# Performance work log

Measured on AMD Instinct MI355X. Metric: run time of the kernel, lower is better.

## Reference

```python
import jax, jax.numpy as jnp
import numpy as np

D_MODEL = 256; D_FLOW = 128; D_FFN = 1024
N_HEADS = 8; N_LEVELS = 3; N_POINTS = 4
D_HEAD = D_MODEL // N_HEADS
SHAPES = np.array([[128, 128], [64, 64], [32, 32]], dtype=np.int64)


def setup_inputs():
    key = jax.random.key(0)
    ks = jax.random.split(key, 12)
    N = 2
    LeNin = int((SHAPES[:, 0] * SHAPES[:, 1]).sum())
    Lq = int(SHAPES[0, 0] * SHAPES[0, 1])
    lsi = np.concatenate([[0], np.cumsum(SHAPES[:, 0] * SHAPES[:, 1])[:-1]])
    s = 0.02
    return {
        'src': jax.random.normal(ks[0], (N, LeNin, D_MODEL), jnp.float32),
        'flow': jax.random.normal(ks[1], (N, Lq, D_FLOW), jnp.float32),
        'spatial_shapes': jnp.asarray(SHAPES, jnp.int32),
        'level_start_index': jnp.asarray(lsi, jnp.int32),
        'w_value': jax.random.normal(ks[2], (D_MODEL, D_MODEL), jnp.float32) * s,
        'b_value': jnp.zeros((D_MODEL,), jnp.float32),
        'w_off': jax.random.normal(ks[3], (D_FLOW, N_HEADS * N_LEVELS * N_POINTS * 2), jnp.float32) * s,
        'b_off': jax.random.normal(ks[4], (N_HEADS * N_LEVELS * N_POINTS * 2,), jnp.float32) * 0.5,
        'w_attn': jax.random.normal(ks[5], (D_FLOW, N_HEADS * N_LEVELS * N_POINTS), jnp.float32) * s,
        'b_attn': jnp.zeros((N_HEADS * N_LEVELS * N_POINTS,), jnp.float32),
        'w_out': jax.random.normal(ks[6], (D_MODEL, D_MODEL), jnp.float32) * s,
        'b_out': jnp.zeros((D_MODEL,), jnp.float32),
        'gamma': jnp.ones((D_MODEL,), jnp.float32),
        'beta': jnp.zeros((D_MODEL,), jnp.float32),
        'w1': jax.random.normal(ks[7], (D_MODEL, D_FFN), jnp.float32) * s,
        'b1': jnp.zeros((D_FFN,), jnp.float32),
        'w2': jax.random.normal(ks[8], (D_FFN, D_MODEL), jnp.float32) * s,
        'b2': jnp.zeros((D_MODEL,), jnp.float32),
    }


def _bilinear_level(v, xy, H, W):
    # v: [N, nh, H*W, dh]; xy: [N, Lq, nh, np, 2] normalized to [0,1]
    # grid_sample(align_corners=False) semantics: pixel = loc * size - 0.5, zero padding
    N, Lq = xy.shape[0], xy.shape[1]
    x = xy[..., 0] * W - 0.5
    y = xy[..., 1] * H - 0.5
    x0 = jnp.floor(x); y0 = jnp.floor(y)
    dx = x - x0; dy = y - y0
    acc = jnp.zeros((N, N_HEADS, Lq * N_POINTS, v.shape[-1]), v.dtype)
    corners = ((x0, y0, (1 - dx) * (1 - dy)),
               (x0 + 1, y0, dx * (1 - dy)),
               (x0, y0 + 1, (1 - dx) * dy),
               (x0 + 1, y0 + 1, dx * dy))
    for ix, iy, w in corners:
        valid = (ix >= 0) & (ix <= W - 1) & (iy >= 0) & (iy <= H - 1)
        xi = jnp.clip(ix, 0, W - 1).astype(jnp.int32)
        yi = jnp.clip(iy, 0, H - 1).astype(jnp.int32)
        idx = (yi * W + xi).transpose(0, 2, 1, 3).reshape(N, N_HEADS, Lq * N_POINTS)
        g = jnp.take_along_axis(v, idx[..., None], axis=2)  # [N, nh, Lq*np, dh]
        wv = (w * valid).transpose(0, 2, 1, 3).reshape(N, N_HEADS, Lq * N_POINTS, 1)
        acc = acc + wv * g
    return acc


def reference(src, flow, spatial_shapes, level_start_index, w_value, b_value,
              w_off, b_off, w_attn, b_attn, w_out, b_out, gamma, beta, w1, b1, w2, b2):
    ss = np.asarray(jax.device_get(spatial_shapes))
    lsi = np.asarray(jax.device_get(level_start_index))
    N, LeNin, _ = src.shape
    Lq = flow.shape[1]
    value = (src @ w_value + b_value).reshape(N, LeNin, N_HEADS, D_HEAD)
    off = (flow @ w_off + b_off).reshape(N, Lq, N_HEADS, N_LEVELS, N_POINTS, 2)
    attn = jax.nn.softmax((flow @ w_attn + b_attn).reshape(N, Lq, N_HEADS, N_LEVELS * N_POINTS), axis=-1)
    attn = attn.reshape(N, Lq, N_HEADS, N_LEVELS, N_POINTS)
    # reference points on level-0 grid (valid_ratios == 1)
    H0, W0 = int(ss[0, 0]), int(ss[0, 1])
    ry, rx = jnp.meshgrid(jnp.linspace(0.5, H0 - 0.5, H0) / H0,
                          jnp.linspace(0.5, W0 - 0.5, W0) / W0, indexing='ij')
    ref = jnp.stack([rx.reshape(-1), ry.reshape(-1)], -1)  # [Lq, 2] (x, y)
    norm = jnp.asarray(np.stack([ss[:, 1], ss[:, 0]], -1), jnp.float32)  # [nl, 2] = (W, H)
    loc = ref[None, :, None, None, None, :] + off / norm[None, None, None, :, None, :]
    acc = jnp.zeros((N, Lq, N_HEADS, D_HEAD), src.dtype)
    for l in range(N_LEVELS):
        H, W = int(ss[l, 0]), int(ss[l, 1])
        st = int(lsi[l])
        v = value[:, st:st + H * W].transpose(0, 2, 1, 3)  # [N, nh, HW, dh]
        s_l = _bilinear_level(v, loc[:, :, :, l], H, W).reshape(N, N_HEADS, Lq, N_POINTS, D_HEAD)
        acc = acc + jnp.einsum('bhqpd,bqhp->bqhd', s_l, attn[:, :, :, l])
    src2 = acc.reshape(N, Lq, D_MODEL) @ w_out + b_out
    x = src2  # dropout is identity at inference
    mu = x.mean(-1, keepdims=True)
    var = ((x - mu) ** 2).mean(-1, keepdims=True)
    ln = (x - mu) / jnp.sqrt(var + 1e-5) * gamma + beta
    ffn = jax.nn.relu(ln @ w1 + b1) @ w2 + b2
    return x + ffn
```

## Files before the change

### kernel.cpp

```cpp
#include <hip/hip_runtime.h>
#include <cstdint>
#include <cstddef>

#define D_MODEL  256
#define D_FLOW   128
#define D_FFN    1024
#define N_HEADS  8
#define N_LEVELS 3
#define N_POINTS 4
#define D_HEAD   32
#define LQ       16384
#define LENIN    21504
#define NB       2

typedef unsigned short ushort;
typedef __attribute__((ext_vector_type(8))) short bf16x8;
typedef __attribute__((ext_vector_type(4))) float f32x4;

__device__ __forceinline__ ushort f2b(float f) {
    uint32_t u = __float_as_uint(f);
    uint32_t r = (u + 0x7fffu + ((u >> 16) & 1u)) >> 16;
    return (ushort)r;
}

__device__ __forceinline__ void gl_lds16(const void* g, void* l) {
    __builtin_amdgcn_global_load_lds(
        (const __attribute__((address_space(1))) unsigned int*)g,
        (__attribute__((address_space(3))) unsigned int*)l,
        16, 0, 0);
}

template<bool A_FP32, bool RELU, bool RESID, bool OUT_BF16>
__global__ __launch_bounds__(256)
void mfma_gemm(const void* __restrict__ Ain, const ushort* __restrict__ Bt,
               const float* __restrict__ bias, const float* __restrict__ resid,
               void* __restrict__ Cout, int N, int K)
{
    __shared__ ushort As[128 * 64];
    __shared__ ushort Bs[128 * 64];

    const int tid  = threadIdx.x;
    const int wave = tid >> 6;
    const int lane = tid & 63;
    const int quad = lane >> 4;
    const int l16  = lane & 15;
    const int wr   = (wave >> 1) * 64;
    const int wc   = (wave & 1) * 64;

    const int nx = gridDim.x;
    int lin = blockIdx.y * nx + blockIdx.x;
    const int total = nx * gridDim.y;
    if ((total & 7) == 0) lin = (lin & 7) * (total >> 3) + (lin >> 3);
    const int by = lin / nx;
    const int bx = lin - by * nx;
    const int bm = by * 128;
    const int bn = bx * 128;

    const int sr  = lane >> 3;
    const int sc  = lane & 7;
    const int gch = sc ^ sr;

    f32x4 acc[4][4] = {};
    const int swz = l16 & 7;

    for (int k0 = 0; k0 < K; k0 += 64) {
        __syncthreads();
        if (A_FP32) {
            const float* Af = (const float*)Ain;
#pragma unroll
            for (int i = 0; i < 4; ++i) {
                const int row = wave * 32 + i * 8 + sr;
                const float* p = Af + (size_t)(bm + row) * K + k0 + gch * 8;
                const float4 v0 = *(const float4*)(p);
                const float4 v1 = *(const float4*)(p + 4);
                bf16x8 pk;
                pk[0] = (short)f2b(v0.x); pk[1] = (short)f2b(v0.y);
                pk[2] = (short)f2b(v0.z); pk[3] = (short)f2b(v0.w);
                pk[4] = (short)f2b(v1.x); pk[5] = (short)f2b(v1.y);
                pk[6] = (short)f2b(v1.z); pk[7] = (short)f2b(v1.w);
                *(bf16x8*)&As[(size_t)row * 64 + sc * 8] = pk;
            }
        } else {
            const ushort* Ab = (const ushort*)Ain;
#pragma unroll
            for (int i = 0; i < 4; ++i) {
                const int row = wave * 32 + i * 8;
                gl_lds16(Ab + (size_t)(bm + row + sr) * K + k0 + gch * 8,
                         As + (size_t)row * 64);
            }
        }
#pragma unroll
        for (int i = 0; i < 4; ++i) {
            const int row = wave * 32 + i * 8;
            gl_lds16(Bt + (size_t)(bn + row + sr) * K + k0 + gch * 8,
                     Bs + (size_t)row * 64);
        }
        __syncthreads();

#pragma unroll
        for (int kk = 0; kk < 2; ++kk) {
            bf16x8 af[4], bfr[4];
#pragma unroll
            for (int mi = 0; mi < 4; ++mi) {
                const int p = (kk * 4 + quad) ^ swz;
                af[mi] = *(const bf16x8*)&As[(wr + mi * 16 + l16) * 64 + p * 8];
            }
#pragma unroll
            for (int ni = 0; ni < 4; ++ni) {
                const int p = (kk * 4 + quad) ^ swz;
                bfr[ni] = *(const bf16x8*)&Bs[(wc + ni * 16 + l16) * 64 + p * 8];
            }
#pragma unroll
            for (int mi = 0; mi < 4; ++mi)
#pragma unroll
                for (int ni = 0; ni < 4; ++ni)
                    acc[mi][ni] = __builtin_amdgcn_mfma_f32_16x16x32_bf16(
                        af[mi], bfr[ni], acc[mi][ni], 0, 0, 0);
        }
    }

#pragma unroll
    for (int mi = 0; mi < 4; ++mi) {
#pragma unroll
        for (int ni = 0; ni < 4; ++ni) {
            const int col = bn + wc + ni * 16 + l16;
            const float bb = bias[col];
#pragma unroll
            for (int r = 0; r < 4; ++r) {
                const int row = bm + wr + mi * 16 + quad * 4 + r;
                const size_t idx = (size_t)row * N + col;
                float c = acc[mi][ni][r] + bb;
                if (RELU)  c = fmaxf(c, 0.f);
                if (RESID) c += resid[idx];
                if (OUT_BF16) ((ushort*)Cout)[idx] = f2b(c);
                else          ((float*)Cout)[idx]  = c;
            }
        }
    }
}

__global__ __launch_bounds__(256)
void gemm_ln_k(const ushort* __restrict__ A, const ushort* __restrict__ Bt,
               const float* __restrict__ bias, const float* __restrict__ gamma,
               const float* __restrict__ beta,
               float* __restrict__ xout, ushort* __restrict__ lnout, int K)
{
    __shared__ ushort As[64 * 32];
    __shared__ ushort Bs[256 * 32];
    __shared__ float  sS[64][33];
    __shared__ float  sS2[64][33];
    __shared__ float  sMu[64], sRi[64];

    const int tid  = threadIdx.x;
    const int wave = tid >> 6;
    const int lane = tid & 63;
    const int quad = lane >> 4;
    const int l16  = lane & 15;
    const int wr   = (wave >> 1) * 32;
    const int wc   = (wave & 1) * 128;
    const int bm   = blockIdx.x * 64;

    const int sr  = lane >> 2;
    const int sc  = lane & 3;
    const int gch = sc ^ (sr & 3);

    f32x4 acc[2][8] = {};
    const int swz = l16 & 3;

    for (int k0 = 0; k0 < K; k0 += 32) {
        __syncthreads();
        gl_lds16(A + (size_t)(bm + wave * 16 + sr) * K + k0 + gch * 8,
                 As + wave * 16 * 32);
#pragma unroll
        for (int i = 0; i < 4; ++i) {
            const int row = wave * 64 + i * 16;
            gl_lds16(Bt + (size_t)(row + sr) * K + k0 + gch * 8,
                     Bs + (size_t)row * 32);
        }
        __syncthreads();

        bf16x8 af[2], bfr[8];
#pragma unroll
        for (int mi = 0; mi < 2; ++mi)
            af[mi] = *(const bf16x8*)&As[(wr + mi * 16 + l16) * 32 + ((quad ^ swz) << 3)];
#pragma unroll
        for (int ni = 0; ni < 8; ++ni)
            bfr[ni] = *(const bf16x8*)&Bs[(wc + ni * 16 + l16) * 32 + ((quad ^ swz) << 3)];
#pragma unroll
        for (int mi = 0; mi < 2; ++mi)
#pragma unroll
            for (int ni = 0; ni < 8; ++ni)
                acc[mi][ni] = __builtin_amdgcn_mfma_f32_16x16x32_bf16(
                    af[mi], bfr[ni], acc[mi][ni], 0, 0, 0);
    }

    float bias8[8], g8[8], b8[8];
#pragma unroll
    for (int ni = 0; ni < 8; ++ni) {
        const int col = wc + ni * 16 + l16;
        bias8[ni] = bias[col];
        g8[ni]    = gamma[col];
        b8[ni]    = beta[col];
    }

#pragma unroll
    for (int mi = 0; mi < 2; ++mi)
#pragma unroll
        for (int r = 0; r < 4; ++r) {
            float s = 0.f, s2 = 0.f;
#pragma unroll
            for (int ni = 0; ni < 8; ++ni) {
                const float c = acc[mi][ni][r] + bias8[ni];
                s += c; s2 += c * c;
            }
            const int row = wr + mi * 16 + quad * 4 + r;
            sS[row][(wave & 1) * 16 + l16]  = s;
            sS2[row][(wave & 1) * 16 + l16] = s2;
        }
    __syncthreads();

    if (tid < 64) {
        float s = 0.f, s2 = 0.f;
#pragma unroll
        for (int j = 0; j < 32; ++j) { s += sS[tid][j]; s2 += sS2[tid][j]; }
        const float mu  = s * (1.f / 256.f);
        const float var = s2 * (1.f / 256.f) - mu * mu;
        sMu[tid] = mu;
        sRi[tid] = rsqrtf(var + 1e-5f);
    }
    __syncthreads();

#pragma unroll
    for (int mi = 0; mi < 2; ++mi)
#pragma unroll
        for (int r = 0; r < 4; ++r) {
            const int lrow = wr + mi * 16 + quad * 4 + r;
            const int grow = bm + lrow;
            const float mu = sMu[lrow], ri = sRi[lrow];
#pragma unroll
            for (int ni = 0; ni < 8; ++ni) {
                const int col = wc + ni * 16 + l16;
                const float c = acc[mi][ni][r] + bias8[ni];
                xout[(size_t)grow * 256 + col]  = c;
                lnout[(size_t)grow * 256 + col] = f2b((c - mu) * ri * g8[ni] + b8[ni]);
            }
        }
}

__global__ __launch_bounds__(512, 3)
void ffn_fused_k(const ushort* __restrict__ ln, const ushort* __restrict__ w1T,
                 const ushort* __restrict__ w2C, const float* __restrict__ b1v,
                 const float* __restrict__ b2v, float* __restrict__ out)
{
    __shared__ ushort smem[29696];
    ushort* const w1s0 = smem;
    ushort* const w1s1 = smem + 8192;
    ushort* const w2s  = smem + 16384;
    ushort* const hS0  = smem + 24576;
    ushort* const hS1  = smem + 27136;
    ushort* const lnS  = smem + 8192;

    const int tid  = threadIdx.x;
    const int wave = tid >> 6;
    const int lane = tid & 63;
    const int quad = lane >> 4;
    const int l16  = lane & 15;
    const int g1m  = wave >> 1;
    const int g1n  = wave & 1;
    const int wm   = wave >> 2;
    const int wn   = wave & 3;
    const int bm   = blockIdx.x * 64;

    const int sr2  = lane >> 5, sc32 = lane & 31;
    const int sr4  = lane >> 2, sc4  = lane & 3;

#pragma unroll
    for (int i = 0; i < 4; ++i) {
        const int r0 = (wave * 4 + i) * 2;
        const int r  = r0 + sr2;
        gl_lds16(ln + (size_t)(bm + r) * 256 + ((sc32 ^ (r & 7)) << 3),
                 lnS + r0 * 256);
    }
#pragma unroll
    for (int i = 0; i < 2; ++i) {
        const int r0 = (wave * 2 + i) * 2;
        const int r  = r0 + sr2;
        gl_lds16(w1T + (size_t)r * 256 + ((sc32 ^ (r & 7)) << 3),
                 w1s0 + r0 * 256);
    }
    __syncthreads();

    bf16x8 afA[8];
#pragma unroll
    for (int kk = 0; kk < 8; ++kk)
        afA[kk] = *(const bf16x8*)&lnS[(g1m * 16 + l16) * 256
                                        + (((kk * 4 + quad) ^ (l16 & 7)) << 3)];
    __syncthreads();

    f32x4 acc2[2][4] = {};

#pragma unroll 1
    for (int c = 0; c < 32; ++c) {
        ushort* const w1cur = (c & 1) ? w1s1 : w1s0;
        ushort* const w1nxt = (c & 1) ? w1s0 : w1s1;
        ushort* const hcur  = (c & 1) ? hS1  : hS0;

        if (c < 31) {
#pragma unroll
            for (int i = 0; i < 2; ++i) {
                const int r0 = (wave * 2 + i) * 2;
                const int r  = r0 + sr2;
                gl_lds16(w1T + (size_t)((c + 1) * 32 + r) * 256
                             + ((sc32 ^ (r & 7)) << 3),
                         w1nxt + r0 * 256);
            }
        }
        {
            const ushort* w2c = w2C + (size_t)c * 8192;
#pragma unroll
            for (int i = 0; i < 2; ++i) {
                const int n0 = (wave * 2 + i) * 16;
                const int rw = n0 + sr4;
                gl_lds16(w2c + (size_t)rw * 32 + ((sc4 ^ ((rw >> 1) & 3)) << 3),
                         w2s + n0 * 32);
            }
        }

        f32x4 acc1 = {};
#pragma unroll
        for (int kk = 0; kk < 8; ++kk) {
            const bf16x8 bf = *(const bf16x8*)&w1cur[(g1n * 16 + l16) * 256
                                   + (((kk * 4 + quad) ^ (l16 & 7)) << 3)];
            acc1 = __builtin_amdgcn_mfma_f32_16x16x32_bf16(afA[kk], bf, acc1, 0, 0, 0);
        }

        {
            const int kc = g1n * 16 + l16;
            const float bb = b1v[c * 32 + kc];
            const int hr = g1m * 16 + quad * 4;
#pragma unroll
            for (int r = 0; r < 4; ++r)
                hcur[(hr + r) * 40 + kc] = f2b(fmaxf(acc1[r] + bb, 0.f));
        }
        __syncthreads();

        {
            bf16x8 a2[2], b2f[4];
#pragma unroll
            for (int mi = 0; mi < 2; ++mi)
                a2[mi] = *(const bf16x8*)&hcur[(wm * 32 + mi * 16 + l16) * 40
                                               + (quad << 3)];
#pragma unroll
            for (int ni = 0; ni < 4; ++ni) {
                const int row = wn * 64 + ni * 16 + l16;
                b2f[ni] = *(const bf16x8*)&w2s[row * 32
                              + ((quad ^ ((l16 >> 1) & 3)) << 3)];
            }
#pragma unroll
            for (int mi = 0; mi < 2; ++mi)
#pragma unroll
                for (int ni = 0; ni < 4; ++ni)
                    acc2[mi][ni] = __builtin_amdgcn_mfma_f32_16x16x32_bf16(
                        a2[mi], b2f[ni], acc2[mi][ni], 0, 0, 0);
        }
        __syncthreads();
    }

#pragma unroll
    for (int ni = 0; ni < 4; ++ni) {
        const int col = wn * 64 + ni * 16 + l16;
        const float bb = b2v[col];
#pragma unroll
        for (int mi = 0; mi < 2; ++mi)
#pragma unroll
            for (int r = 0; r < 4; ++r) {
                const int row = bm + wm * 32 + mi * 16 + quad * 4 + r;
                const size_t idx = (size_t)row * 256 + col;
                out[idx] = out[idx] + acc2[mi][ni][r] + bb;
            }
    }
}

__device__ __forceinline__ void acc8(float* a, uint4 g, float w) {
    a[0] = fmaf(w, __uint_as_float(g.x << 16), a[0]);
    a[1] = fmaf(w, __uint_as_float(g.x), a[1]);
    a[2] = fmaf(w, __uint_as_float(g.y << 16), a[2]);
    a[3] = fmaf(w, __uint_as_float(g.y), a[3]);
    a[4] = fmaf(w, __uint_as_float(g.z << 16), a[4]);
    a[5] = fmaf(w, __uint_as_float(g.z), a[5]);
    a[6] = fmaf(w, __uint_as_float(g.w << 16), a[6]);
    a[7] = fmaf(w, __uint_as_float(g.w), a[7]);
}

__global__ __launch_bounds__(256)
void sample_k(const ushort* __restrict__ value, const ushort* __restrict__ projc,
              ushort* __restrict__ acc)
{
    __shared__ float sOff[8][192];
    __shared__ float sAttn[8][96];

    const int tid = threadIdx.x;
    const int bid = blockIdx.x;
    const int bq0 = (((bid & 7) << 9) | (bid >> 3)) << 3;

    for (int i = tid; i < 8 * 288; i += 256) {
        const int qw = i / 288, j = i - qw * 288;
        const float v = __uint_as_float((uint32_t)projc[(size_t)(bq0 + qw) * 384 + j] << 16);
        if (j < 192) sOff[qw][j] = v;
        else         sAttn[qw][j - 192] = v;
    }
    __syncthreads();

    if (tid < 64) {
        const int qw = tid >> 3, h = tid & 7;
        float* row = &sAttn[qw][h * 12];
        float m = row[0];
#pragma unroll
        for (int j = 1; j < 12; ++j) m = fmaxf(m, row[j]);
        float s = 0.f;
#pragma unroll
        for (int j = 0; j < 12; ++j) { const float e = __expf(row[j] - m); row[j] = e; s += e; }
        const float inv = 1.f / s;
#pragma unroll
        for (int j = 0; j < 12; ++j) row[j] *= inv;
    }
    __syncthreads();

    const int wave = tid >> 6, lane = tid & 63;
    const int qh = lane >> 5;
    const int h  = (lane >> 2) & 7;
    const int cg = lane & 3;
    const int qw = wave * 2 + qh;
    const int bq = bq0 + qw;
    const int n  = bq >> 14;
    const int q  = bq & 16383;

    const float qx = (float)(q & 127) + 0.5f;
    const float qy = (float)(q >> 7) + 0.5f;

    const int LSIc[3] = {0, 16384, 20480};

    float a[8] = {0.f, 0.f, 0.f, 0.f, 0.f, 0.f, 0.f, 0.f};
    const ushort* vbase = value + (size_t)n * LENIN * D_MODEL + h * D_HEAD + cg * 8;

#pragma unroll
    for (int l = 0; l < N_LEVELS; ++l) {
        const int   W     = 128 >> l;
        const int   SH    = 7 - l;
        const float scale = 1.f / (float)(1 << l);
        const float cx    = qx * scale - 0.5f;
        const float cy    = qy * scale - 0.5f;
        const ushort* vlev = vbase + ((size_t)LSIc[l] << 8);
#pragma unroll
        for (int p = 0; p < N_POINTS; ++p) {
            const int ob = (h * N_LEVELS + l) * (N_POINTS * 2) + p * 2;
            const float aw = sAttn[qw][h * 12 + l * 4 + p];
            const float x = cx + sOff[qw][ob];
            const float y = cy + sOff[qw][ob + 1];
            const float x0f = floorf(x), y0f = floorf(y);
            const int x0 = (int)x0f, y0 = (int)y0f;
            const float dx = x - x0f, dy = y - y0f;
            float wx1 = dx * aw, wx0 = aw - wx1;
            float wy1 = dy,      wy0 = 1.f - dy;
            if ((unsigned)x0       > (unsigned)(W - 1)) wx0 = 0.f;
            if ((unsigned)(x0 + 1) > (unsigned)(W - 1)) wx1 = 0.f;
            if ((unsigned)y0       > (unsigned)(W - 1)) wy0 = 0.f;
            if ((unsigned)(y0 + 1) > (unsigned)(W - 1)) wy1 = 0.f;
            const int xi0 = min(max(x0, 0), W - 1);
            const int xi1 = min(max(x0 + 1, 0), W - 1);
            const int yi0 = min(max(y0, 0), W - 1);
            const int yi1 = min(max(y0 + 1, 0), W - 1);
            const uint4 g00 = *(const uint4*)(vlev + ((size_t)((yi0 << SH) + xi0) << 8));
            const uint4 g01 = *(const uint4*)(vlev + ((size_t)((yi0 << SH) + xi1) << 8));
            const uint4 g10 = *(const uint4*)(vlev + ((size_t)((yi1 << SH) + xi0) << 8));
            const uint4 g11 = *(const uint4*)(vlev + ((size_t)((yi1 << SH) + xi1) << 8));
            acc8(a, g00, wx0 * wy0);
            acc8(a, g01, wx1 * wy0);
            acc8(a, g10, wx0 * wy1);
            acc8(a, g11, wx1 * wy1);
        }
    }

    const uint32_t o0 = (uint32_t)f2b(a[0]) | ((uint32_t)f2b(a[1]) << 16);
    const uint32_t o1 = (uint32_t)f2b(a[2]) | ((uint32_t)f2b(a[3]) << 16);
    const uint32_t o2 = (uint32_t)f2b(a[4]) | ((uint32_t)f2b(a[5]) << 16);
    const uint32_t o3 = (uint32_t)f2b(a[6]) | ((uint32_t)f2b(a[7]) << 16);
    const uint4 ov = {o0, o1, o2, o3};
    *(uint4*)(acc + (size_t)bq * D_MODEL + h * D_HEAD + cg * 8) = ov;
}

__global__ __launch_bounds__(256)
void prep_all_k(const float* __restrict__ w_value, const float* __restrict__ w_out,
                const float* __restrict__ w1, const float* __restrict__ w2,
                const float* __restrict__ w_off, const float* __restrict__ b_off,
                const float* __restrict__ w_attn, const float* __restrict__ b_attn,
                ushort* __restrict__ wvT, ushort* __restrict__ woT,
                ushort* __restrict__ w1T, ushort* __restrict__ w2C,
                ushort* __restrict__ wcT, float* __restrict__ biasc)
{
    int i = blockIdx.x * 256 + threadIdx.x;
    if (i < 65536) {
        const int k = i >> 8, n = i & 255;
        wvT[(size_t)n * 256 + k] = f2b(w_value[i]);
        return;
    }
    i -= 65536;
    if (i < 65536) {
        const int k = i >> 8, n = i & 255;
        woT[(size_t)n * 256 + k] = f2b(w_out[i]);
        return;
    }
    i -= 65536;
    if (i < 262144) {
        const int k = i >> 10, n = i & 1023;
        w1T[(size_t)n * 256 + k] = f2b(w1[i]);
        return;
    }
    i -= 262144;
    if (i < 262144) {
        const int k = i >> 8, n = i & 255;
        w2C[(size_t)(k >> 5) * 8192 + n * 32 + (k & 31)] = f2b(w2[i]);
        return;
    }
    i -= 262144;
    if (i < 49152) {
        const int nn = i >> 7, k = i & 127;
        float v = 0.f;
        if (nn < 192)      v = w_off[(size_t)k * 192 + nn];
        else if (nn < 288) v = w_attn[(size_t)k * 96 + (nn - 192)];
        wcT[i] = f2b(v);
        return;
    }
    i -= 49152;
    if (i < 384) {
        float b = 0.f;
        if (i < 192)      b = b_off[i];
        else if (i < 288) b = b_attn[i - 192];
        biasc[i] = b;
    }
}

extern "C" void kernel_launch(void* const* d_in, const int* in_sizes, int n_in,
                              void* d_out, int out_size, void* d_ws, size_t ws_size,
                              hipStream_t stream)
{
    const float* src     = (const float*)d_in[0];
    const float* flow    = (const float*)d_in[1];
    const float* w_value = (const float*)d_in[4];
    const float* b_value = (const float*)d_in[5];
    const float* w_off   = (const float*)d_in[6];
    const float* b_off   = (const float*)d_in[7];
    const float* w_attn  = (const float*)d_in[8];
    const float* b_attn  = (const float*)d_in[9];
    const float* w_out   = (const float*)d_in[10];
    const float* b_out   = (const float*)d_in[11];
    const float* gamma   = (const float*)d_in[12];
    const float* beta    = (const float*)d_in[13];
    const float* w1      = (const float*)d_in[14];
    const float* b1      = (const float*)d_in[15];
    const float* w2      = (const float*)d_in[16];
    const float* b2      = (const float*)d_in[17];
    float* out = (float*)d_out;
    char*  wsb = (char*)d_ws;

    ushort* value_bf = (ushort*)(wsb);
    ushort* acc_bf   = (ushort*)(wsb + 22020096);
    ushort* projc_bf = (ushort*)(wsb + 67108864);
    ushort* ln_bf    = (ushort*)(wsb + 67108864);
    ushort* wvT      = (ushort*)(wsb + 92274688);
    ushort* woT      = (ushort*)(wsb + 92405760);
    ushort* w1T      = (ushort*)(wsb + 92536832);
    ushort* w2C      = (ushort*)(wsb + 93061120);
    ushort* wcT      = (ushort*)(wsb + 93585408);
    float*  biasc    = (float*) (wsb + 93683712);

    const int Mq = NB * LQ;
    const int Mv = NB * LENIN;

    prep_all_k<<<2754, 256, 0, stream>>>(w_value, w_out, w1, w2,
                                         w_off, b_off, w_attn, b_attn,
                                         wvT, woT, w1T, w2C, wcT, biasc);

    mfma_gemm<true, false, false, true><<<dim3(2, Mv / 128), 256, 0, stream>>>(
        src, wvT, b_value, nullptr, value_bf, 256, 256);

    mfma_gemm<true, false, false, true><<<dim3(3, Mq / 128), 256, 0, stream>>>(
        flow, wcT, biasc, nullptr, projc_bf, 384, 128);

    sample_k<<<Mq / 8, 256, 0, stream>>>(value_bf, projc_bf, acc_bf);

    gemm_ln_k<<<Mq / 64, 256, 0, stream>>>(
        acc_bf, woT, b_out, gamma, beta, out, ln_bf, 256);

    ffn_fused_k<<<Mq / 64, 512, 0, stream>>>(ln_bf, w1T, w2C, b1, b2, out);
}
```

Baseline: 270.6 us.

## Warp-specialize fused FFN into producer/consumer waves with 128-row tiles

Restructures the fused FFN kernel so four waves compute the first GEMM (hidden chunk with ReLU) while the other four accumulate the second GEMM on the previous chunk, software-pipelined with double-buffered hidden and W2 tiles. The row tile grows from 64 to 128, halving the grid and the number of passes over the weights, and each consumer wave now holds a 32x256 accumulator. This trades higher register pressure (launch_bounds minimum-occupancy hint dropped), more LDS, and fewer blocks for better weight reuse and overlap between the two GEMMs.

```diff
diff --git a/kernel.cpp b/kernel.cpp
--- a/kernel.cpp
+++ b/kernel.cpp
@@ -247,137 +247,182 @@
         }
 }
 
-__global__ __launch_bounds__(512, 3)
+__global__ __launch_bounds__(512)
 void ffn_fused_k(const ushort* __restrict__ ln, const ushort* __restrict__ w1T,
                  const ushort* __restrict__ w2C, const float* __restrict__ b1v,
                  const float* __restrict__ b2v, float* __restrict__ out)
 {
-    __shared__ ushort smem[29696];
-    ushort* const w1s0 = smem;
-    ushort* const w1s1 = smem + 8192;
-    ushort* const w2s  = smem + 16384;
-    ushort* const hS0  = smem + 24576;
-    ushort* const hS1  = smem + 27136;
-    ushort* const lnS  = smem + 8192;
+    __shared__ ushort smem[32768];
+    ushort* const w1s  = smem;
+    ushort* const w2s0 = smem + 8192;
+    ushort* const w2s1 = smem + 16384;
+    ushort* const hs0  = smem + 24576;
+    ushort* const hs1  = smem + 28672;
+    ushort* const lnS  = smem;
 
     const int tid  = threadIdx.x;
     const int wave = tid >> 6;
     const int lane = tid & 63;
     const int quad = lane >> 4;
     const int l16  = lane & 15;
-    const int g1m  = wave >> 1;
-    const int g1n  = wave & 1;
-    const int wm   = wave >> 2;
-    const int wn   = wave & 3;
-    const int bm   = blockIdx.x * 64;
-
-    const int sr2  = lane >> 5, sc32 = lane & 31;
-    const int sr4  = lane >> 2, sc4  = lane & 3;
-
-#pragma unroll
-    for (int i = 0; i < 4; ++i) {
-        const int r0 = (wave * 4 + i) * 2;
-        const int r  = r0 + sr2;
-        gl_lds16(ln + (size_t)(bm + r) * 256 + ((sc32 ^ (r & 7)) << 3),
+    const int bm   = blockIdx.x * 128;
+    const bool producer = (wave < 4);
+
+#pragma unroll
+    for (int i = 0; i < 8; ++i) {
+        const int r0 = (wave * 8 + i) * 2;
+        const int r  = r0 + (lane >> 5);
+        gl_lds16(ln + (size_t)(bm + r) * 256 + (((lane & 31) ^ (r & 7)) << 3),
                  lnS + r0 * 256);
     }
+    __syncthreads();
+
+    bf16x8 afA[2][8];
+    if (producer) {
+#pragma unroll
+        for (int mi = 0; mi < 2; ++mi)
+#pragma unroll
+            for (int kk = 0; kk < 8; ++kk) {
+                const int row = wave * 32 + mi * 16 + l16;
+                afA[mi][kk] = *(const bf16x8*)
+                    &lnS[row * 256 + ((((kk * 4 + quad)) ^ (row & 7)) << 3)];
+            }
+    }
+    __syncthreads();
+
 #pragma unroll
     for (int i = 0; i < 2; ++i) {
         const int r0 = (wave * 2 + i) * 2;
-        const int r  = r0 + sr2;
-        gl_lds16(w1T + (size_t)r * 256 + ((sc32 ^ (r & 7)) << 3),
-                 w1s0 + r0 * 256);
+        const int r  = r0 + (lane >> 5);
+        gl_lds16(w1T + (size_t)r * 256 + (((lane & 31) ^ (r & 7)) << 3),
+                 w1s + r0 * 256);
     }
     __syncthreads();
 
-    bf16x8 afA[8];
-#pragma unroll
-    for (int kk = 0; kk < 8; ++kk)
-        afA[kk] = *(const bf16x8*)&lnS[(g1m * 16 + l16) * 256
-                                        + (((kk * 4 + quad) ^ (l16 & 7)) << 3)];
-    __syncthreads();
-
-    f32x4 acc2[2][4] = {};
+    f32x4 acc2[2][16] = {};
 
 #pragma unroll 1
-    for (int c = 0; c < 32; ++c) {
-        ushort* const w1cur = (c & 1) ? w1s1 : w1s0;
-        ushort* const w1nxt = (c & 1) ? w1s0 : w1s1;
-        ushort* const hcur  = (c & 1) ? hS1  : hS0;
+    for (int c = 0; c <= 32; ++c) {
+        f32x4 acc1[2][2];
+        bf16x8 a2[2];
+
+        if (c < 32) {
+            const ushort* src = w2C + (size_t)c * 8192;
+            ushort* dst = (c & 1) ? w2s1 : w2s0;
+#pragma unroll
+            for (int i = 0; i < 2; ++i) {
+                const int r0 = (wave * 2 + i) * 16;
+                const int r  = r0 + (lane >> 2);
+                gl_lds16(src + (size_t)r * 32 + (((lane & 3) ^ ((r >> 2) & 3)) << 3),
+                         dst + r0 * 32);
+            }
+        }
+
+        if (producer) {
+            if (c < 32) {
+#pragma unroll
+                for (int mi = 0; mi < 2; ++mi)
+#pragma unroll
+                    for (int nj = 0; nj < 2; ++nj)
+                        acc1[mi][nj] = f32x4{0.f, 0.f, 0.f, 0.f};
+#pragma unroll
+                for (int kk = 0; kk < 8; ++kk) {
+#pragma unroll
+                    for (int nj = 0; nj < 2; ++nj) {
+                        const int brow = nj * 16 + l16;
+                        const bf16x8 bf = *(const bf16x8*)
+                            &w1s[brow * 256 + (((kk * 4 + quad) ^ (brow & 7)) << 3)];
+                        acc1[0][nj] = __builtin_amdgcn_mfma_f32_16x16x32_bf16(
+                            afA[0][kk], bf, acc1[0][nj], 0, 0, 0);
+                        acc1[1][nj] = __builtin_amdgcn_mfma_f32_16x16x32_bf16(
+                            afA[1][kk], bf, acc1[1][nj], 0, 0, 0);
+                    }
+                }
+            }
+        } else if (c >= 1) {
+            const ushort* hp  = (c & 1) ? hs0 : hs1;
+            const ushort* w2p = (c & 1) ? w2s0 : w2s1;
+            const int qq = wave - 4;
+#pragma unroll
+            for (int mi = 0; mi < 2; ++mi) {
+                const int row = qq * 32 + mi * 16 + l16;
+                a2[mi] = *(const bf16x8*)
+                    &hp[row * 32 + ((quad ^ ((row >> 2) & 3)) << 3)];
+            }
+#pragma unroll
+            for (int nt = 0; nt < 8; ++nt) {
+                const int brow = nt * 16 + l16;
+                const bf16x8 b2 = *(const bf16x8*)
+                    &w2p[brow * 32 + ((quad ^ ((brow >> 2) & 3)) << 3)];
+                acc2[0][nt] = __builtin_amdgcn_mfma_f32_16x16x32_bf16(
+                    a2[0], b2, acc2[0][nt], 0, 0, 0);
+                acc2[1][nt] = __builtin_amdgcn_mfma_f32_16x16x32_bf16(
+                    a2[1], b2, acc2[1][nt], 0, 0, 0);
+            }
+        }
+        __syncthreads();
 
         if (c < 31) {
 #pragma unroll
             for (int i = 0; i < 2; ++i) {
                 const int r0 = (wave * 2 + i) * 2;
-                const int r  = r0 + sr2;
+                const int r  = r0 + (lane >> 5);
                 gl_lds16(w1T + (size_t)((c + 1) * 32 + r) * 256
-                             + ((sc32 ^ (r & 7)) << 3),
-                         w1nxt + r0 * 256);
-            }
-        }
-        {
-            const ushort* w2c = w2C + (size_t)c * 8192;
-#pragma unroll
-            for (int i = 0; i < 2; ++i) {
-                const int n0 = (wave * 2 + i) * 16;
-                const int rw = n0 + sr4;
-                gl_lds16(w2c + (size_t)rw * 32 + ((sc4 ^ ((rw >> 1) & 3)) << 3),
-                         w2s + n0 * 32);
-            }
-        }
-
-        f32x4 acc1 = {};
-#pragma unroll
-        for (int kk = 0; kk < 8; ++kk) {
-            const bf16x8 bf = *(const bf16x8*)&w1cur[(g1n * 16 + l16) * 256
-                                   + (((kk * 4 + quad) ^ (l16 & 7)) << 3)];
-            acc1 = __builtin_amdgcn_mfma_f32_16x16x32_bf16(afA[kk], bf, acc1, 0, 0, 0);
-        }
-
-        {
-            const int kc = g1n * 16 + l16;
-            const float bb = b1v[c * 32 + kc];
-            const int hr = g1m * 16 + quad * 4;
-#pragma unroll
-            for (int r = 0; r < 4; ++r)
-                hcur[(hr + r) * 40 + kc] = f2b(fmaxf(acc1[r] + bb, 0.f));
+                             + (((lane & 31) ^ (r & 7)) << 3),
+                         w1s + r0 * 256);
+            }
+        }
+
+        if (producer) {
+            if (c < 32) {
+                ushort* hw = (c & 1) ? hs1 : hs0;
+                const float bb0 = b1v[c * 32 + l16];
+                const float bb1 = b1v[c * 32 + 16 + l16];
+#pragma unroll
+                for (int mi = 0; mi < 2; ++mi)
+#pragma unroll
+                    for (int nj = 0; nj < 2; ++nj) {
+                        const int k = nj * 16 + l16;
+                        const float bb = nj ? bb1 : bb0;
+#pragma unroll
+                        for (int r = 0; r < 4; ++r) {
+                            const int row = wave * 32 + mi * 16 + quad * 4 + r;
+                            hw[row * 32 + (((k >> 3) ^ ((row >> 2) & 3)) << 3)
+                                 + (k & 7)] = f2b(fmaxf(acc1[mi][nj][r] + bb, 0.f));
+                        }
+                    }
+            }
+        } else if (c >= 1) {
+            const ushort* w2p = (c & 1) ? w2s0 : w2s1;
+#pragma unroll
+            for (int nt = 8; nt < 16; ++nt) {
+                const int brow = nt * 16 + l16;
+                const bf16x8 b2 = *(const bf16x8*)
+                    &w2p[brow * 32 + ((quad ^ ((brow >> 2) & 3)) << 3)];
+                acc2[0][nt] = __builtin_amdgcn_mfma_f32_16x16x32_bf16(
+                    a2[0], b2, acc2[0][nt], 0, 0, 0);
+                acc2[1][nt] = __builtin_amdgcn_mfma_f32_16x16x32_bf16(
+                    a2[1], b2, acc2[1][nt], 0, 0, 0);
+            }
         }
         __syncthreads();
-
-        {
-            bf16x8 a2[2], b2f[4];
+    }
+
+    if (!producer) {
+        const int qq = wave - 4;
+#pragma unroll
+        for (int nt = 0; nt < 16; ++nt) {
+            const int col = nt * 16 + l16;
+            const float bb = b2v[col];
 #pragma unroll
             for (int mi = 0; mi < 2; ++mi)
-                a2[mi] = *(const bf16x8*)&hcur[(wm * 32 + mi * 16 + l16) * 40
-                                               + (quad << 3)];
-#pragma unroll
-            for (int ni = 0; ni < 4; ++ni) {
-                const int row = wn * 64 + ni * 16 + l16;
-                b2f[ni] = *(const bf16x8*)&w2s[row * 32
-                              + ((quad ^ ((l16 >> 1) & 3)) << 3)];
-            }
-#pragma unroll
-            for (int mi = 0; mi < 2; ++mi)
-#pragma unroll
-                for (int ni = 0; ni < 4; ++ni)
-                    acc2[mi][ni] = __builtin_amdgcn_mfma_f32_16x16x32_bf16(
-                        a2[mi], b2f[ni], acc2[mi][ni], 0, 0, 0);
-        }
-        __syncthreads();
-    }
-
-#pragma unroll
-    for (int ni = 0; ni < 4; ++ni) {
-        const int col = wn * 64 + ni * 16 + l16;
-        const float bb = b2v[col];
-#pragma unroll
-        for (int mi = 0; mi < 2; ++mi)
-#pragma unroll
-            for (int r = 0; r < 4; ++r) {
-                const int row = bm + wm * 32 + mi * 16 + quad * 4 + r;
-                const size_t idx = (size_t)row * 256 + col;
-                out[idx] = out[idx] + acc2[mi][ni][r] + bb;
-            }
+#pragma unroll
+                for (int r = 0; r < 4; ++r) {
+                    const int row = bm + qq * 32 + mi * 16 + quad * 4 + r;
+                    const size_t idx = (size_t)row * 256 + col;
+                    out[idx] = out[idx] + acc2[mi][nt][r] + bb;
+                }
+        }
     }
 }
 
@@ -592,5 +637,5 @@
     gemm_ln_k<<<Mq / 64, 256, 0, stream>>>(
         acc_bf, woT, b_out, gamma, beta, out, ln_bf, 256);
 
-    ffn_fused_k<<<Mq / 64, 512, 0, stream>>>(ln_bf, w1T, w2C, b1, b2, out);
-}
+    ffn_fused_k<<<Mq / 128, 512, 0, stream>>>(ln_bf, w1T, w2C, b1, b2, out);
+}
```

Result: slower. 282.8 us (+4.5%).
